# Optimization experiments

Measured on AMD Instinct MI355X. Metric: run time of the kernel, lower is better.

Reference implementation:

```python
import jax, jax.numpy as jnp
import numpy as np
import math

D_MODEL = 768
N_HEADS = 12
D_HEAD = D_MODEL // N_HEADS
B, T = 2, 2048


def setup_inputs() -> dict:
    key = jax.random.key(0)
    k1, k2, k3, k4, k5 = jax.random.split(key, 5)
    x = jax.random.normal(k1, (B, T, D_MODEL), dtype=jnp.float32)
    # mask == 1 means masked (masked_fill). Causal: mask upper triangle.
    mask = jnp.triu(jnp.ones((T, T), dtype=jnp.int32), k=1)[None, None]  # [1,1,T,T]
    # qkv Linear: weight [3*d_model, d_model], bias [3*d_model]
    lim_qkv = 1.0 / math.sqrt(D_MODEL)
    W_qkv = jax.random.uniform(k2, (3 * D_MODEL, D_MODEL), minval=-lim_qkv, maxval=lim_qkv, dtype=jnp.float32)
    b_qkv = jax.random.uniform(k3, (3 * D_MODEL,), minval=-lim_qkv, maxval=lim_qkv, dtype=jnp.float32)
    W_proj = jax.random.uniform(k4, (D_MODEL, D_MODEL), minval=-lim_qkv, maxval=lim_qkv, dtype=jnp.float32)
    b_proj = jax.random.uniform(k5, (D_MODEL,), minval=-lim_qkv, maxval=lim_qkv, dtype=jnp.float32)
    return {"x": x, "mask": mask, "W_qkv": W_qkv, "b_qkv": b_qkv, "W_proj": W_proj, "b_proj": b_proj}


def reference(x, mask, W_qkv, b_qkv, W_proj, b_proj):
    Bx, Tx, C = x.shape
    qkv = x @ W_qkv.T + b_qkv                      # [B,T,3C]
    q, k, v = jnp.split(qkv, 3, axis=-1)
    # [B,T,H,Dh] -> [B,H,T,Dh]
    q = q.reshape(Bx, Tx, N_HEADS, D_HEAD).transpose(0, 2, 1, 3)
    k = k.reshape(Bx, Tx, N_HEADS, D_HEAD).transpose(0, 2, 1, 3)
    v = v.reshape(Bx, Tx, N_HEADS, D_HEAD).transpose(0, 2, 1, 3)
    att = jnp.einsum('bhqd,bhkd->bhqk', q, k) / math.sqrt(D_HEAD)
    att = jnp.where(mask == 1, -jnp.inf, att)
    att = jax.nn.softmax(att, axis=-1)
    out = jnp.einsum('bhqk,bhkd->bhqd', att, v)    # [B,H,T,Dh]
    out = out.transpose(0, 2, 1, 3).reshape(Bx, Tx, C)
    return out @ W_proj.T + b_proj
```

## Files before the change

kernel.cpp:

```cpp
#include <hip/hip_runtime.h>
#include <hip/hip_bf16.h>
#include <cstdint>

#define D_MODEL 768
#define N_HEADS 12
#define D_HEAD  64
#define BATCH   2
#define SEQ     2048
#define NQ64    (SEQ / 64)
#define SCALE_Q 0.18033688011112042f
#define NSL     4
#define NBH     (BATCH * N_HEADS)

typedef float f32x4 __attribute__((ext_vector_type(4)));
typedef short s16x8 __attribute__((ext_vector_type(8)));
typedef short s16x4 __attribute__((ext_vector_type(4)));
typedef unsigned short u16;

static __device__ __forceinline__ u16 f2bf(float f) {
    union { float f; unsigned int u; } c; c.f = f;
    unsigned int u = c.u;
    u += 0x7fffu + ((u >> 16) & 1u);
    return (u16)(u >> 16);
}
static __device__ __forceinline__ float b2f(u16 u) {
    union { unsigned u; float f; } c; c.u = ((unsigned)u) << 16; return c.f;
}
static __device__ __forceinline__ float e2(float x) {
#if __has_builtin(__builtin_amdgcn_exp2f)
    return __builtin_amdgcn_exp2f(x);
#else
    return exp2f(x);
#endif
}
static __device__ __forceinline__ s16x4 pk4(float p0, float p1, float p2, float p3) {
    union { __hip_bfloat162 h[2]; s16x4 v; } u;
    u.h[0] = __float22bfloat162_rn(make_float2(p0, p1));
    u.h[1] = __float22bfloat162_rn(make_float2(p2, p3));
    return u.v;
}

static __device__ __forceinline__ f32x4 mfma16x32(s16x8 a, s16x8 b, f32x4 c) {
    return __builtin_amdgcn_mfma_f32_16x16x32_bf16(a, b, c, 0, 0, 0);
}
static __device__ __forceinline__ f32x4 mfma16x16(s16x4 a, s16x4 b, f32x4 c) {
#if __has_builtin(__builtin_amdgcn_mfma_f32_16x16x16bf16_1k)
    return __builtin_amdgcn_mfma_f32_16x16x16bf16_1k(a, b, c, 0, 0, 0);
#else
    asm volatile("v_mfma_f32_16x16x16_bf16 %0, %1, %2, %0" : "+v"(c) : "v"(a), "v"(b));
    return c;
#endif
}
static __device__ __forceinline__ void gload_lds16(const void* g, void* l) {
    __builtin_amdgcn_global_load_lds(
        (const __attribute__((address_space(1))) unsigned int*)g,
        (__attribute__((address_space(3))) unsigned int*)l, 16, 0, 0);
}

__global__ __launch_bounds__(256)
void cvt3_kernel(const float* __restrict__ s0, u16* __restrict__ d0, int n0,
                 const float* __restrict__ s1, u16* __restrict__ d1, int n1,
                 const float* __restrict__ s2, u16* __restrict__ d2, int n2)
{
    const int idx4 = (blockIdx.x * 256 + threadIdx.x) * 4;
    const float* s; u16* d; int local;
    if (idx4 < n0)           { s = s0; d = d0; local = idx4; }
    else if (idx4 < n0 + n1) { s = s1; d = d1; local = idx4 - n0; }
    else if (idx4 < n0 + n1 + n2) { s = s2; d = d2; local = idx4 - n0 - n1; }
    else return;
    float4 v = *(const float4*)(s + local);
    ushort4 o;
    o.x = f2bf(v.x); o.y = f2bf(v.y); o.z = f2bf(v.z); o.w = f2bf(v.w);
    *(ushort4*)(d + local) = o;
}

template<int BM, int BN, int MODE>
__global__ __launch_bounds__(256)
void mfma_gemm_kernel(const u16* __restrict__ A, const u16* __restrict__ Bw,
                      const float* __restrict__ bias,
                      float* __restrict__ outf,
                      u16* __restrict__ qo, u16* __restrict__ ko, u16* __restrict__ vt,
                      int M, int N, int K)
{
    constexpr int BK = 32;
    __shared__ u16 As[BM * BK];
    __shared__ u16 Bs[BN * BK];
    const int tid = threadIdx.x;
    const int wave = tid >> 6, lane = tid & 63;
    const int wr = wave >> 1, wc = wave & 1;
    constexpr int WM = BM / 2, WN = BN / 2, FI = WM / 16, FJ = WN / 16;
    const int g = lane >> 4, c = lane & 15;
    const int bm = blockIdx.x * BM, bn = blockIdx.y * BN;

    f32x4 acc[FI][FJ] = {};

    constexpr int IA = (BM * BK * 2) / (256 * 16);
    constexpr int IB = (BN * BK * 2) / (256 * 16);

    const u16* asrc[IA]; const u16* bsrc[IB];
    #pragma unroll
    for (int i = 0; i < IA; ++i) {
        const int idx = tid + i * 256;
        const int row = idx >> 2, kc = idx & 3;
        const int kcs = kc ^ ((row >> 1) & 3);
        asrc[i] = A + (size_t)(bm + row) * K + kcs * 8;
    }
    #pragma unroll
    for (int i = 0; i < IB; ++i) {
        const int idx = tid + i * 256;
        const int row = idx >> 2, kc = idx & 3;
        const int kcs = kc ^ ((row >> 1) & 3);
        bsrc[i] = Bw + (size_t)(bn + row) * K + kcs * 8;
    }
    const int gsw = g ^ ((c >> 1) & 3);

    for (int k0 = 0; k0 < K; k0 += BK) {
        if (k0) __syncthreads();
        #pragma unroll
        for (int i = 0; i < IA; ++i) gload_lds16(asrc[i] + k0, &As[(tid + i * 256) * 8]);
        #pragma unroll
        for (int i = 0; i < IB; ++i) gload_lds16(bsrc[i] + k0, &Bs[(tid + i * 256) * 8]);
        __syncthreads();

        s16x8 af[FI], bfr[FJ];
        #pragma unroll
        for (int i = 0; i < FI; ++i)
            af[i] = *(const s16x8*)&As[(wr * WM + i * 16 + c) * BK + gsw * 8];
        #pragma unroll
        for (int j = 0; j < FJ; ++j)
            bfr[j] = *(const s16x8*)&Bs[(wc * WN + j * 16 + c) * BK + gsw * 8];
        #pragma unroll
        for (int i = 0; i < FI; ++i)
            #pragma unroll
            for (int j = 0; j < FJ; ++j)
                acc[i][j] = mfma16x32(af[i], bfr[j], acc[i][j]);
    }

    if (MODE == 1) {
        #pragma unroll
        for (int j = 0; j < FJ; ++j) {
            const int col = bn + wc * WN + j * 16 + c;
            const float bv = bias[col];
            #pragma unroll
            for (int i = 0; i < FI; ++i) {
                const int row0 = bm + wr * WM + i * 16 + g * 4;
                #pragma unroll
                for (int r = 0; r < 4; ++r)
                    outf[(size_t)(row0 + r) * N + col] = acc[i][j][r] + bv;
            }
        }
    } else {
        const int which = bn / D_MODEL;
        #pragma unroll
        for (int j = 0; j < FJ; ++j) {
            const int gcol = bn + wc * WN + j * 16 + c;
            const float bv = bias[gcol];
            const int scol = gcol - which * D_MODEL;
            const int h = scol >> 6, d = scol & 63;
            if (which == 2) {
                #pragma unroll
                for (int i = 0; i < FI; ++i) {
                    const int row0 = bm + wr * WM + i * 16 + g * 4;
                    const int b = row0 >> 11, t = row0 & 2047;
                    ushort4 pv;
                    pv.x = f2bf(acc[i][j][0] + bv);
                    pv.y = f2bf(acc[i][j][1] + bv);
                    pv.z = f2bf(acc[i][j][2] + bv);
                    pv.w = f2bf(acc[i][j][3] + bv);
                    *(ushort4*)(vt + ((size_t)(b * N_HEADS + h) * 64 + d) * SEQ + t) = pv;
                }
            } else {
                u16* dst = (which == 0) ? qo : ko;
                const float sc = (which == 0) ? SCALE_Q : 1.0f;
                #pragma unroll
                for (int i = 0; i < FI; ++i) {
                    const int row0 = bm + wr * WM + i * 16 + g * 4;
                    const int b = row0 >> 11, t = row0 & 2047;
                    #pragma unroll
                    for (int r = 0; r < 4; ++r)
                        dst[(((size_t)(b * N_HEADS + h) * SEQ + t + r) << 6) + d] =
                            f2bf((acc[i][j][r] + bv) * sc);
                }
            }
        }
    }
}

__global__ __launch_bounds__(256, 3)
void mfma_attn_kernel(const u16* __restrict__ qb, const u16* __restrict__ kb,
                      const u16* __restrict__ vtb, u16* __restrict__ ob,
                      u16* __restrict__ pO, float* __restrict__ pML)
{
    __shared__ __align__(16) u16 OL[NSL][64][64];
    __shared__ float ML[NSL][2][64];
    const int tid = threadIdx.x;
    const int lane = tid & 63;
    const int s = tid >> 6;
    const int blk = blockIdx.x;
    const int bh = blk % NBH;
    const int u = blk / NBH;
    int jblk, half, nparts;
    if (u < 16) { jblk = 15 - u;          half = 0;          nparts = 1; }
    else        { const int uu = u - 16;  jblk = 31 - (uu >> 1); half = uu & 1; nparts = 2; }

    const int ntt = 4 * (jblk + 1);
    const int hl  = ntt / nparts;
    const int w0  = half * hl;
    const int t0  = w0 + (hl * s) / 4;
    const int t1  = w0 + (hl * (s + 1)) / 4;
    const int jq0 = 4 * jblk;

    const int g = lane >> 4, c = lane & 15;
    const int rbase = g << 2;
    const int q0 = jblk << 6;

    s16x8 qa0[4], qa1[4];
    #pragma unroll
    for (int qq = 0; qq < 4; ++qq) {
        const u16* qp = qb + ((size_t)bh * SEQ + q0 + qq * 16 + c) * 64 + g * 8;
        qa0[qq] = *(const s16x8*)(qp);
        qa1[qq] = *(const s16x8*)(qp + 32);
    }

    f32x4 o[4][4] = {};
    float m[4] = {0.f, 0.f, 0.f, 0.f};
    float l[4] = {0.f, 0.f, 0.f, 0.f};

#define TILEQ(QQ, CK0, CK1, CV0, CV1, CV2, CV3, MASKED) {                         \
    f32x4 sa = {0,0,0,0}, sb = {0,0,0,0};                                         \
    sa = mfma16x32(CK0, qa0[QQ], sa);                                             \
    sb = mfma16x32(CK1, qa1[QQ], sb);                                             \
    f32x4 sv = sa + sb;                                                           \
    if (MASKED) {                                                                 \
        if (rbase + 0 > c) sv[0] = -1e30f;                                        \
        if (rbase + 1 > c) sv[1] = -1e30f;                                        \
        if (rbase + 2 > c) sv[2] = -1e30f;                                        \
        if (rbase + 3 > c) sv[3] = -1e30f;                                        \
    }                                                                             \
    float pmax = fmaxf(fmaxf(sv[0], sv[1]), fmaxf(sv[2], sv[3]));                 \
    if (__any(pmax > m[QQ] + 8.f)) {                      \
        pmax = fmaxf(pmax, __shfl_xor(pmax, 16));                                 \
        pmax = fmaxf(pmax, __shfl_xor(pmax, 32));                                 \
        const float mn = fmaxf(m[QQ], pmax);                                      \
        const float scr = e2(m[QQ] - mn);                                         \
        l[QQ] *= scr;                                                             \
        f32x4 scv;                                                                \
        scv[0] = __shfl(scr, rbase + 0);                                          \
        scv[1] = __shfl(scr, rbase + 1);                                          \
        scv[2] = __shfl(scr, rbase + 2);                                          \
        scv[3] = __shfl(scr, rbase + 3);                                          \
        o[QQ][0] *= scv; o[QQ][1] *= scv; o[QQ][2] *= scv; o[QQ][3] *= scv;       \
        m[QQ] = mn;                                                               \
    }                                                                             \
    const float p0 = e2(sv[0] - m[QQ]), p1 = e2(sv[1] - m[QQ]);                   \
    const float p2 = e2(sv[2] - m[QQ]), p3 = e2(sv[3] - m[QQ]);                   \
    l[QQ] += (p0 + p1) + (p2 + p3);                                               \
    const s16x4 pa = pk4(p0, p1, p2, p3);                                         \
    o[QQ][0] = mfma16x16(pa, CV0, o[QQ][0]);                                      \
    o[QQ][1] = mfma16x16(pa, CV1, o[QQ][1]);                                      \
    o[QQ][2] = mfma16x16(pa, CV2, o[QQ][2]);                                      \
    o[QQ][3] = mfma16x16(pa, CV3, o[QQ][3]);                                      \
}

    {
        const u16* kp = kb + (size_t)bh * SEQ * 64 + c * 64 + g * 8 + (size_t)t0 * 1024;
        const u16* vp = vtb + ((size_t)bh * 64 + c) * SEQ + g * 4 + t0 * 16;

        s16x8 ck0 = *(const s16x8*)(kp);
        s16x8 ck1 = *(const s16x8*)(kp + 32);
        s16x4 cv0 = *(const s16x4*)(vp);
        s16x4 cv1 = *(const s16x4*)(vp + 16 * SEQ);
        s16x4 cv2 = *(const s16x4*)(vp + 32 * SEQ);
        s16x4 cv3 = *(const s16x4*)(vp + 48 * SEQ);

        for (int t = t0; t < t1; ++t) {
            kp += 1024; vp += 16;
            const s16x8 nk0 = *(const s16x8*)(kp);
            const s16x8 nk1 = *(const s16x8*)(kp + 32);
            const s16x4 nv0 = *(const s16x4*)(vp);
            const s16x4 nv1 = *(const s16x4*)(vp + 16 * SEQ);
            const s16x4 nv2 = *(const s16x4*)(vp + 32 * SEQ);
            const s16x4 nv3 = *(const s16x4*)(vp + 48 * SEQ);

            #pragma unroll
            for (int qq = 0; qq < 4; ++qq) {
                if (t <= jq0 + qq) {
                    TILEQ(qq, ck0, ck1, cv0, cv1, cv2, cv3, (t == jq0 + qq));
                }
            }
            ck0 = nk0; ck1 = nk1;
            cv0 = nv0; cv1 = nv1; cv2 = nv2; cv3 = nv3;
        }
    }
#undef TILEQ

    u16* OLs = &OL[s][0][0];
    #pragma unroll
    for (int qq = 0; qq < 4; ++qq) {
        float lt = l[qq] + __shfl_xor(l[qq], 16);
        lt += __shfl_xor(lt, 32);
        #pragma unroll
        for (int r = 0; r < 4; ++r) {
            const int row = qq * 16 + rbase + r;
            #pragma unroll
            for (int j = 0; j < 4; ++j) {
                const int col = c + 16 * j;
                const int idx = row * 64 + ((((col >> 3) ^ (row & 7)) << 3) | (col & 7));
                OLs[idx] = f2bf(o[qq][j][r]);
            }
        }
        if (g == 0) {
            ML[s][0][qq * 16 + c] = m[qq];
            ML[s][1][qq * 16 + c] = lt;
        }
    }
    __syncthreads();

    {
        const int row = tid >> 2;
        const int cq = (tid & 3) << 4;
        float mv[NSL], lv[NSL];
        float mm = -3.0e38f;
        #pragma unroll
        for (int sp = 0; sp < NSL; ++sp) {
            mv[sp] = ML[sp][0][row];
            lv[sp] = ML[sp][1][row];
            mm = fmaxf(mm, mv[sp]);
        }
        float w[NSL], denom = 0.f;
        #pragma unroll
        for (int sp = 0; sp < NSL; ++sp) {
            w[sp] = e2(mv[sp] - mm);
            denom += lv[sp] * w[sp];
        }

        float a[16] = {};
        #pragma unroll
        for (int sp = 0; sp < NSL; ++sp) {
            const float ws = w[sp];
            #pragma unroll
            for (int h2 = 0; h2 < 2; ++h2) {
                const int ch = (cq >> 3) + h2;
                const int idx = row * 64 + ((ch ^ (row & 7)) << 3);
                const uint4 xv = *(const uint4*)&OL[sp][0][idx];
                a[h2 * 8 + 0] += ws * b2f((u16)(xv.x & 0xffff));
                a[h2 * 8 + 1] += ws * b2f((u16)(xv.x >> 16));
                a[h2 * 8 + 2] += ws * b2f((u16)(xv.y & 0xffff));
                a[h2 * 8 + 3] += ws * b2f((u16)(xv.y >> 16));
                a[h2 * 8 + 4] += ws * b2f((u16)(xv.z & 0xffff));
                a[h2 * 8 + 5] += ws * b2f((u16)(xv.z >> 16));
                a[h2 * 8 + 6] += ws * b2f((u16)(xv.w & 0xffff));
                a[h2 * 8 + 7] += ws * b2f((u16)(xv.w >> 16));
            }
        }

        if (nparts == 1) {
            const float inv = 1.0f / denom;
            const int b = bh / N_HEADS, h = bh % N_HEADS;
            const int t = (jblk << 6) + row;
            u16* dst = ob + ((size_t)b * SEQ + t) * D_MODEL + h * 64 + cq;
            #pragma unroll
            for (int e4 = 0; e4 < 4; ++e4) {
                ushort4 ov;
                ov.x = f2bf(a[e4 * 4 + 0] * inv);
                ov.y = f2bf(a[e4 * 4 + 1] * inv);
                ov.z = f2bf(a[e4 * 4 + 2] * inv);
                ov.w = f2bf(a[e4 * 4 + 3] * inv);
                *(ushort4*)(dst + e4 * 4) = ov;
            }
        } else {
            const int ps = (bh * 16 + (jblk - 16)) * 2 + half;
            u16* Od = pO + (size_t)ps * 4096 + row * 64 + cq;
            #pragma unroll
            for (int e4 = 0; e4 < 4; ++e4) {
                ushort4 ov;
                ov.x = f2bf(a[e4 * 4 + 0]);
                ov.y = f2bf(a[e4 * 4 + 1]);
                ov.z = f2bf(a[e4 * 4 + 2]);
                ov.w = f2bf(a[e4 * 4 + 3]);
                *(ushort4*)(Od + e4 * 4) = ov;
            }
            if ((tid & 3) == 0) {
                pML[ps * 128 + row]      = mm;
                pML[ps * 128 + 64 + row] = denom;
            }
        }
    }
}

__global__ __launch_bounds__(256)
void attn_merge_kernel(const u16* __restrict__ pO, const float* __restrict__ pML,
                       u16* __restrict__ ob)
{
    const int blk = blockIdx.x;
    const int bh = blk % NBH;
    const int hj = blk / NBH;
    const int jblk = 16 + hj;
    const int tid = threadIdx.x;
    const int row = tid >> 2;
    const int cq = (tid & 3) << 4;
    const int ps = (bh * 16 + hj) * 2;

    const float m0 = pML[(size_t)ps * 128 + row];
    const float l0 = pML[(size_t)ps * 128 + 64 + row];
    const float m1 = pML[(size_t)(ps + 1) * 128 + row];
    const float l1 = pML[(size_t)(ps + 1) * 128 + 64 + row];
    const float mm = fmaxf(m0, m1);
    const float w0 = e2(m0 - mm), w1 = e2(m1 - mm);
    const float inv = 1.0f / (l0 * w0 + l1 * w1);
    const float a0 = w0 * inv, a1 = w1 * inv;

    const u16* O0 = pO + (size_t)ps * 4096 + row * 64 + cq;
    const u16* O1 = O0 + 4096;
    const int b = bh / N_HEADS, h = bh % N_HEADS;
    const int t = (jblk << 6) + row;
    u16* dst = ob + ((size_t)b * SEQ + t) * D_MODEL + h * 64 + cq;
    #pragma unroll
    for (int e4 = 0; e4 < 4; ++e4) {
        const ushort4 x0 = *(const ushort4*)(O0 + e4 * 4);
        const ushort4 x1 = *(const ushort4*)(O1 + e4 * 4);
        ushort4 ov;
        ov.x = f2bf(a0 * b2f(x0.x) + a1 * b2f(x1.x));
        ov.y = f2bf(a0 * b2f(x0.y) + a1 * b2f(x1.y));
        ov.z = f2bf(a0 * b2f(x0.z) + a1 * b2f(x1.z));
        ov.w = f2bf(a0 * b2f(x0.w) + a1 * b2f(x1.w));
        *(ushort4*)(dst + e4 * 4) = ov;
    }
}

extern "C" void kernel_launch(void* const* d_in, const int* in_sizes, int n_in,
                              void* d_out, int out_size, void* d_ws, size_t ws_size,
                              hipStream_t stream)
{
    const float* x      = (const float*)d_in[0];
    const float* W_qkv  = (const float*)d_in[2];
    const float* b_qkv  = (const float*)d_in[3];
    const float* W_proj = (const float*)d_in[4];
    const float* b_proj = (const float*)d_in[5];
    float* out = (float*)d_out;

    const int nX = BATCH * SEQ * D_MODEL;
    const int nWq = 3 * D_MODEL * D_MODEL;
    const int nWp = D_MODEL * D_MODEL;
    u16* xb  = (u16*)d_ws;
    u16* wqb = xb + nX;
    u16* wpb = wqb + nWq;
    u16* qbf = wpb + nWp;
    u16* kbf = qbf + nX;
    u16* vtb = kbf + nX;
    u16* ao  = vtb + nX;
    u16* pO  = ao + nX;
    float* pML = (float*)(pO + (size_t)768 * 4096);

    const int tot4 = (nX + nWq + nWp) / 4;
    cvt3_kernel<<<(tot4 + 255) / 256, 256, 0, stream>>>(x, xb, nX, W_qkv, wqb, nWq,
                                                        W_proj, wpb, nWp);

    mfma_gemm_kernel<128, 128, 0><<<dim3(32, 18), 256, 0, stream>>>(
        xb, wqb, b_qkv, nullptr, qbf, kbf, vtb, BATCH * SEQ, 3 * D_MODEL, D_MODEL);

    mfma_attn_kernel<<<dim3(48 * NBH), 256, 0, stream>>>(
        qbf, kbf, vtb, ao, pO, pML);
    attn_merge_kernel<<<dim3(16 * NBH), 256, 0, stream>>>(pO, pML, ao);

    mfma_gemm_kernel<128, 64, 1><<<dim3(32, 12), 256, 0, stream>>>(
        ao, wpb, b_proj, out, nullptr, nullptr, nullptr, BATCH * SEQ, D_MODEL, D_MODEL);
}
```

Measured before the change: 103.7 us.

## Balance causal attention work by pairing short and long query blocks per workgroup

Each attention workgroup now processes two query blocks in sequence, block p and block 31-p, each split in half across KV, so every workgroup does roughly equal causal work. This replaces the previous mix of whole short blocks and halved long blocks, and cuts the grid from 48*NBH to 32*NBH workgroups. All query blocks now go through the partial-output path and the merge kernel, which adds partial writes and merge traffic for the short blocks that were previously written directly.

```diff
diff --git a/kernel.cpp b/kernel.cpp
--- a/kernel.cpp
+++ b/kernel.cpp
@@ -188,7 +188,7 @@
 
 __global__ __launch_bounds__(256, 3)
 void mfma_attn_kernel(const u16* __restrict__ qb, const u16* __restrict__ kb,
-                      const u16* __restrict__ vtb, u16* __restrict__ ob,
+                      const u16* __restrict__ vtb,
                       u16* __restrict__ pO, float* __restrict__ pML)
 {
     __shared__ __align__(16) u16 OL[NSL][64][64];
@@ -199,32 +199,10 @@
     const int blk = blockIdx.x;
     const int bh = blk % NBH;
     const int u = blk / NBH;
-    int jblk, half, nparts;
-    if (u < 16) { jblk = 15 - u;          half = 0;          nparts = 1; }
-    else        { const int uu = u - 16;  jblk = 31 - (uu >> 1); half = uu & 1; nparts = 2; }
-
-    const int ntt = 4 * (jblk + 1);
-    const int hl  = ntt / nparts;
-    const int w0  = half * hl;
-    const int t0  = w0 + (hl * s) / 4;
-    const int t1  = w0 + (hl * (s + 1)) / 4;
-    const int jq0 = 4 * jblk;
+    const int p = u >> 1, h = u & 1;
 
     const int g = lane >> 4, c = lane & 15;
     const int rbase = g << 2;
-    const int q0 = jblk << 6;
-
-    s16x8 qa0[4], qa1[4];
-    #pragma unroll
-    for (int qq = 0; qq < 4; ++qq) {
-        const u16* qp = qb + ((size_t)bh * SEQ + q0 + qq * 16 + c) * 64 + g * 8;
-        qa0[qq] = *(const s16x8*)(qp);
-        qa1[qq] = *(const s16x8*)(qp + 32);
-    }
-
-    f32x4 o[4][4] = {};
-    float m[4] = {0.f, 0.f, 0.f, 0.f};
-    float l[4] = {0.f, 0.f, 0.f, 0.f};
 
 #define TILEQ(QQ, CK0, CK1, CV0, CV1, CV2, CV3, MASKED) {                         \
     f32x4 sa = {0,0,0,0}, sb = {0,0,0,0};                                         \
@@ -262,114 +240,122 @@
     o[QQ][3] = mfma16x16(pa, CV3, o[QQ][3]);                                      \
 }
 
-    {
-        const u16* kp = kb + (size_t)bh * SEQ * 64 + c * 64 + g * 8 + (size_t)t0 * 1024;
-        const u16* vp = vtb + ((size_t)bh * 64 + c) * SEQ + g * 4 + t0 * 16;
-
-        s16x8 ck0 = *(const s16x8*)(kp);
-        s16x8 ck1 = *(const s16x8*)(kp + 32);
-        s16x4 cv0 = *(const s16x4*)(vp);
-        s16x4 cv1 = *(const s16x4*)(vp + 16 * SEQ);
-        s16x4 cv2 = *(const s16x4*)(vp + 32 * SEQ);
-        s16x4 cv3 = *(const s16x4*)(vp + 48 * SEQ);
-
-        for (int t = t0; t < t1; ++t) {
-            kp += 1024; vp += 16;
-            const s16x8 nk0 = *(const s16x8*)(kp);
-            const s16x8 nk1 = *(const s16x8*)(kp + 32);
-            const s16x4 nv0 = *(const s16x4*)(vp);
-            const s16x4 nv1 = *(const s16x4*)(vp + 16 * SEQ);
-            const s16x4 nv2 = *(const s16x4*)(vp + 32 * SEQ);
-            const s16x4 nv3 = *(const s16x4*)(vp + 48 * SEQ);
-
-            #pragma unroll
-            for (int qq = 0; qq < 4; ++qq) {
-                if (t <= jq0 + qq) {
-                    TILEQ(qq, ck0, ck1, cv0, cv1, cv2, cv3, (t == jq0 + qq));
+    #pragma unroll 1
+    for (int ph = 0; ph < 2; ++ph) {
+        const int jblk = ph ? (31 - p) : p;
+        const int ntt = 4 * (jblk + 1);
+        const int hl = ntt >> 1;
+        const int w0 = h * hl;
+        const int t0 = w0 + (hl * s) / 4;
+        const int t1 = w0 + (hl * (s + 1)) / 4;
+        const int jq0 = 4 * jblk;
+        const int q0 = jblk << 6;
+
+        s16x8 qa0[4], qa1[4];
+        #pragma unroll
+        for (int qq = 0; qq < 4; ++qq) {
+            const u16* qp = qb + ((size_t)bh * SEQ + q0 + qq * 16 + c) * 64 + g * 8;
+            qa0[qq] = *(const s16x8*)(qp);
+            qa1[qq] = *(const s16x8*)(qp + 32);
+        }
+
+        f32x4 o[4][4] = {};
+        float m[4] = {0.f, 0.f, 0.f, 0.f};
+        float l[4] = {0.f, 0.f, 0.f, 0.f};
+
+        if (t0 < t1) {
+            const u16* kp = kb + (size_t)bh * SEQ * 64 + c * 64 + g * 8 + (size_t)t0 * 1024;
+            const u16* vp = vtb + ((size_t)bh * 64 + c) * SEQ + g * 4 + t0 * 16;
+
+            s16x8 ck0 = *(const s16x8*)(kp);
+            s16x8 ck1 = *(const s16x8*)(kp + 32);
+            s16x4 cv0 = *(const s16x4*)(vp);
+            s16x4 cv1 = *(const s16x4*)(vp + 16 * SEQ);
+            s16x4 cv2 = *(const s16x4*)(vp + 32 * SEQ);
+            s16x4 cv3 = *(const s16x4*)(vp + 48 * SEQ);
+
+            for (int t = t0; t < t1; ++t) {
+                kp += 1024; vp += 16;
+                const s16x8 nk0 = *(const s16x8*)(kp);
+                const s16x8 nk1 = *(const s16x8*)(kp + 32);
+                const s16x4 nv0 = *(const s16x4*)(vp);
+                const s16x4 nv1 = *(const s16x4*)(vp + 16 * SEQ);
+                const s16x4 nv2 = *(const s16x4*)(vp + 32 * SEQ);
+                const s16x4 nv3 = *(const s16x4*)(vp + 48 * SEQ);
+
+                #pragma unroll
+                for (int qq = 0; qq < 4; ++qq) {
+                    if (t <= jq0 + qq) {
+                        TILEQ(qq, ck0, ck1, cv0, cv1, cv2, cv3, (t == jq0 + qq));
+                    }
                 }
-            }
-            ck0 = nk0; ck1 = nk1;
-            cv0 = nv0; cv1 = nv1; cv2 = nv2; cv3 = nv3;
-        }
-    }
-#undef TILEQ
-
-    u16* OLs = &OL[s][0][0];
-    #pragma unroll
-    for (int qq = 0; qq < 4; ++qq) {
-        float lt = l[qq] + __shfl_xor(l[qq], 16);
-        lt += __shfl_xor(lt, 32);
-        #pragma unroll
-        for (int r = 0; r < 4; ++r) {
-            const int row = qq * 16 + rbase + r;
-            #pragma unroll
-            for (int j = 0; j < 4; ++j) {
-                const int col = c + 16 * j;
-                const int idx = row * 64 + ((((col >> 3) ^ (row & 7)) << 3) | (col & 7));
-                OLs[idx] = f2bf(o[qq][j][r]);
-            }
-        }
-        if (g == 0) {
-            ML[s][0][qq * 16 + c] = m[qq];
-            ML[s][1][qq * 16 + c] = lt;
-        }
-    }
-    __syncthreads();
-
-    {
-        const int row = tid >> 2;
-        const int cq = (tid & 3) << 4;
-        float mv[NSL], lv[NSL];
-        float mm = -3.0e38f;
-        #pragma unroll
-        for (int sp = 0; sp < NSL; ++sp) {
-            mv[sp] = ML[sp][0][row];
-            lv[sp] = ML[sp][1][row];
-            mm = fmaxf(mm, mv[sp]);
-        }
-        float w[NSL], denom = 0.f;
-        #pragma unroll
-        for (int sp = 0; sp < NSL; ++sp) {
-            w[sp] = e2(mv[sp] - mm);
-            denom += lv[sp] * w[sp];
-        }
-
-        float a[16] = {};
-        #pragma unroll
-        for (int sp = 0; sp < NSL; ++sp) {
-            const float ws = w[sp];
-            #pragma unroll
-            for (int h2 = 0; h2 < 2; ++h2) {
-                const int ch = (cq >> 3) + h2;
-                const int idx = row * 64 + ((ch ^ (row & 7)) << 3);
-                const uint4 xv = *(const uint4*)&OL[sp][0][idx];
-                a[h2 * 8 + 0] += ws * b2f((u16)(xv.x & 0xffff));
-                a[h2 * 8 + 1] += ws * b2f((u16)(xv.x >> 16));
-                a[h2 * 8 + 2] += ws * b2f((u16)(xv.y & 0xffff));
-                a[h2 * 8 + 3] += ws * b2f((u16)(xv.y >> 16));
-                a[h2 * 8 + 4] += ws * b2f((u16)(xv.z & 0xffff));
-                a[h2 * 8 + 5] += ws * b2f((u16)(xv.z >> 16));
-                a[h2 * 8 + 6] += ws * b2f((u16)(xv.w & 0xffff));
-                a[h2 * 8 + 7] += ws * b2f((u16)(xv.w >> 16));
-            }
-        }
-
-        if (nparts == 1) {
-            const float inv = 1.0f / denom;
-            const int b = bh / N_HEADS, h = bh % N_HEADS;
-            const int t = (jblk << 6) + row;
-            u16* dst = ob + ((size_t)b * SEQ + t) * D_MODEL + h * 64 + cq;
-            #pragma unroll
-            for (int e4 = 0; e4 < 4; ++e4) {
-                ushort4 ov;
-                ov.x = f2bf(a[e4 * 4 + 0] * inv);
-                ov.y = f2bf(a[e4 * 4 + 1] * inv);
-                ov.z = f2bf(a[e4 * 4 + 2] * inv);
-                ov.w = f2bf(a[e4 * 4 + 3] * inv);
-                *(ushort4*)(dst + e4 * 4) = ov;
-            }
-        } else {
-            const int ps = (bh * 16 + (jblk - 16)) * 2 + half;
+                ck0 = nk0; ck1 = nk1;
+                cv0 = nv0; cv1 = nv1; cv2 = nv2; cv3 = nv3;
+            }
+        }
+
+        __syncthreads();
+        u16* OLs = &OL[s][0][0];
+        #pragma unroll
+        for (int qq = 0; qq < 4; ++qq) {
+            float lt = l[qq] + __shfl_xor(l[qq], 16);
+            lt += __shfl_xor(lt, 32);
+            #pragma unroll
+            for (int r = 0; r < 4; ++r) {
+                const int row = qq * 16 + rbase + r;
+                #pragma unroll
+                for (int j = 0; j < 4; ++j) {
+                    const int col = c + 16 * j;
+                    const int idx = row * 64 + ((((col >> 3) ^ (row & 7)) << 3) | (col & 7));
+                    OLs[idx] = f2bf(o[qq][j][r]);
+                }
+            }
+            if (g == 0) {
+                ML[s][0][qq * 16 + c] = m[qq];
+                ML[s][1][qq * 16 + c] = lt;
+            }
+        }
+        __syncthreads();
+
+        {
+            const int row = tid >> 2;
+            const int cq = (tid & 3) << 4;
+            float mv[NSL], lv[NSL];
+            float mm = -3.0e38f;
+            #pragma unroll
+            for (int sp = 0; sp < NSL; ++sp) {
+                mv[sp] = ML[sp][0][row];
+                lv[sp] = ML[sp][1][row];
+                mm = fmaxf(mm, mv[sp]);
+            }
+            float w[NSL], denom = 0.f;
+            #pragma unroll
+            for (int sp = 0; sp < NSL; ++sp) {
+                w[sp] = e2(mv[sp] - mm);
+                denom += lv[sp] * w[sp];
+            }
+
+            float a[16] = {};
+            #pragma unroll
+            for (int sp = 0; sp < NSL; ++sp) {
+                const float ws = w[sp];
+                #pragma unroll
+                for (int h2 = 0; h2 < 2; ++h2) {
+                    const int ch = (cq >> 3) + h2;
+                    const int idx = row * 64 + ((ch ^ (row & 7)) << 3);
+                    const uint4 xv = *(const uint4*)&OL[sp][0][idx];
+                    a[h2 * 8 + 0] += ws * b2f((u16)(xv.x & 0xffff));
+                    a[h2 * 8 + 1] += ws * b2f((u16)(xv.x >> 16));
+                    a[h2 * 8 + 2] += ws * b2f((u16)(xv.y & 0xffff));
+                    a[h2 * 8 + 3] += ws * b2f((u16)(xv.y >> 16));
+                    a[h2 * 8 + 4] += ws * b2f((u16)(xv.z & 0xffff));
+                    a[h2 * 8 + 5] += ws * b2f((u16)(xv.z >> 16));
+                    a[h2 * 8 + 6] += ws * b2f((u16)(xv.w & 0xffff));
+                    a[h2 * 8 + 7] += ws * b2f((u16)(xv.w >> 16));
+                }
+            }
+
+            const int ps = (bh * NQ64 + jblk) * 2 + h;
             u16* Od = pO + (size_t)ps * 4096 + row * 64 + cq;
             #pragma unroll
             for (int e4 = 0; e4 < 4; ++e4) {
@@ -381,11 +367,12 @@
                 *(ushort4*)(Od + e4 * 4) = ov;
             }
             if ((tid & 3) == 0) {
-                pML[ps * 128 + row]      = mm;
-                pML[ps * 128 + 64 + row] = denom;
-            }
-        }
-    }
+                pML[(size_t)ps * 128 + row]      = mm;
+                pML[(size_t)ps * 128 + 64 + row] = denom;
+            }
+        }
+    }
+#undef TILEQ
 }
 
 __global__ __launch_bounds__(256)
@@ -394,12 +381,11 @@
 {
     const int blk = blockIdx.x;
     const int bh = blk % NBH;
-    const int hj = blk / NBH;
-    const int jblk = 16 + hj;
+    const int j = blk / NBH;
     const int tid = threadIdx.x;
     const int row = tid >> 2;
     const int cq = (tid & 3) << 4;
-    const int ps = (bh * 16 + hj) * 2;
+    const int ps = (bh * NQ64 + j) * 2;
 
     const float m0 = pML[(size_t)ps * 128 + row];
     const float l0 = pML[(size_t)ps * 128 + 64 + row];
@@ -413,7 +399,7 @@
     const u16* O0 = pO + (size_t)ps * 4096 + row * 64 + cq;
     const u16* O1 = O0 + 4096;
     const int b = bh / N_HEADS, h = bh % N_HEADS;
-    const int t = (jblk << 6) + row;
+    const int t = (j << 6) + row;
     u16* dst = ob + ((size_t)b * SEQ + t) * D_MODEL + h * 64 + cq;
     #pragma unroll
     for (int e4 = 0; e4 < 4; ++e4) {
@@ -450,7 +436,7 @@
     u16* vtb = kbf + nX;
     u16* ao  = vtb + nX;
     u16* pO  = ao + nX;
-    float* pML = (float*)(pO + (size_t)768 * 4096);
+    float* pML = (float*)(pO + (size_t)NBH * NQ64 * 2 * 4096);
 
     const int tot4 = (nX + nWq + nWp) / 4;
     cvt3_kernel<<<(tot4 + 255) / 256, 256, 0, stream>>>(x, xb, nX, W_qkv, wqb, nWq,
@@ -459,9 +445,9 @@
     mfma_gemm_kernel<128, 128, 0><<<dim3(32, 18), 256, 0, stream>>>(
         xb, wqb, b_qkv, nullptr, qbf, kbf, vtb, BATCH * SEQ, 3 * D_MODEL, D_MODEL);
 
-    mfma_attn_kernel<<<dim3(48 * NBH), 256, 0, stream>>>(
-        qbf, kbf, vtb, ao, pO, pML);
-    attn_merge_kernel<<<dim3(16 * NBH), 256, 0, stream>>>(pO, pML, ao);
+    mfma_attn_kernel<<<dim3(NQ64 * NBH), 256, 0, stream>>>(
+        qbf, kbf, vtb, pO, pML);
+    attn_merge_kernel<<<dim3(NQ64 * NBH), 256, 0, stream>>>(pO, pML, ao);
 
     mfma_gemm_kernel<128, 64, 1><<<dim3(32, 12), 256, 0, stream>>>(
         ao, wpb, b_proj, out, nullptr, nullptr, nullptr, BATCH * SEQ, D_MODEL, D_MODEL);
```

Measured after the change: 120.9 us. 16.6% more time.
